# Kernel optimization log

Hardware: AMD Instinct MI355X
Metric: run time of the kernel (lower is better)

Reference implementation:

```python
import jax, jax.numpy as jnp
import numpy as np

B, C, H, W, L = 2, 64, 48, 48, 48
GH, GW, GL = 24, 24, 24  # gating signal at half resolution


def setup_inputs() -> dict:
    key = jax.random.key(0)
    k = jax.random.split(key, 6)
    x = jax.random.normal(k[0], (B, C, H, W, L), dtype=jnp.float32)
    g = jax.random.normal(k[1], (B, C, GH, GW, GL), dtype=jnp.float32)
    s = 1.0 / np.sqrt(C)
    W1 = jax.random.normal(k[2], (C, C), dtype=jnp.float32) * s  # conv1 1x1x1 weight (out,in)
    b1 = jax.random.normal(k[3], (C,), dtype=jnp.float32) * 0.01
    W2 = jax.random.normal(k[4], (C, C), dtype=jnp.float32) * s  # conv2 1x1x1 weight
    b2 = jax.random.normal(k[5], (C,), dtype=jnp.float32) * 0.01
    return {"x": x, "g": g, "W1": W1, "b1": b1, "W2": W2, "b2": b2}


def _conv1x1(v, Wm, b):
    # 1x1x1 Conv3d == channel-mixing matmul
    return jnp.einsum('bchwl,oc->bohwl', v, Wm) + b[None, :, None, None, None]


def reference(x, g, W1, b1, W2, b2):
    theta_x = _conv1x1(x, W1, b1)                       # (B, C, H, W, L)
    theta_g = _conv1x1(g, W2, b2)                       # (B, C, GH, GW, GL)
    # F.upsample(mode='trilinear', align_corners=False) -> half-pixel trilinear resize
    theta_g = jax.image.resize(theta_g, (B, C, H, W, L), method='trilinear')

    # spatially-normalized elementwise gate
    theta_c = theta_x * theta_g
    theta_c = theta_c - jnp.min(theta_c)                # global min over whole tensor
    theta_c = theta_c / jnp.sum(theta_c, axis=(2, 3, 4), keepdims=True)
    p = theta_c * x

    # channel-channel attention per (b,h,w), contracting over L
    theta_c_d = jnp.einsum('bihwl,bjhwl->bhwij', theta_x, theta_g)  # (B,H,W,C,C)
    theta_c_d = theta_c_d - jnp.min(theta_c_d)
    theta_c_d = theta_c_d / jnp.sum(theta_c_d, axis=(1, 2, 3, 4), keepdims=True)
    d = jnp.einsum('bchwl,bhwcj->bjhwl', x, theta_c_d)  # (B, C, H, W, L)
    return (p, d)
```

## Files before the change

### kernel.cpp

```cpp
#include <hip/hip_runtime.h>

#define Bb 2
#define Cc 64
#define Hh 48
#define Ww 48
#define Ll 48
#define HWc (Hh*Ww)
#define HWL (HWc*Ll)
#define GHh 24
#define SG (GHh*GHh*GHh)
#define NBLK (Bb*HWc)
#define CNT1f 110592.0f
#define CNT2f 9437184.0f

__device__ __forceinline__ void interp1(int i, int& a, int& b, float& f){
  float src = i*0.5f - 0.25f;
  float fl = floorf(src);
  f = src - fl;
  int i0 = (int)fl;
  a = i0 < 0 ? 0 : i0;
  int i1 = i0 + 1;
  b = i1 > (GHh-1) ? (GHh-1) : i1;
}

__device__ __forceinline__ void ltaps(int l, int& a, int& b, float& f){
  int i0 = (l - 1) >> 1;
  a = i0 < 0 ? 0 : i0;
  b = i0 + 1 > 23 ? 23 : i0 + 1;
  f = (l & 1) ? 0.25f : 0.75f;
}

__global__ __launch_bounds__(256) void conv_k(const float* __restrict__ in,
    const float* __restrict__ Wm, const float* __restrict__ bias,
    float* __restrict__ out, int S){
  __shared__ __align__(16) float Wl[64][68];
  __shared__ __align__(16) float xl[64][68];
  int t = threadIdx.x;
  int ntile = S >> 6;
  int b  = blockIdx.x / ntile;
  int s0 = (blockIdx.x % ntile) << 6;
  for (int q = t; q < 4096; q += 256){
    int o = q >> 6, c = q & 63;
    Wl[c][o] = Wm[q];
  }
  const float* inb = in + (size_t)b*Cc*S + s0;
  for (int q = t; q < 1024; q += 256){
    int c = q >> 4, v = (q & 15) << 2;
    float4 val = *(const float4*)(inb + (size_t)c*S + v);
    *(float4*)&xl[c][v] = val;
  }
  __syncthreads();
  int o0 = (t & 15) << 2, s1 = (t >> 4) << 2;
  float a00=0,a01=0,a02=0,a03=0,a10=0,a11=0,a12=0,a13=0;
  float a20=0,a21=0,a22=0,a23=0,a30=0,a31=0,a32=0,a33=0;
  #pragma unroll 8
  for (int c = 0; c < 64; ++c){
    float4 wv = *(const float4*)&Wl[c][o0];
    float4 xv = *(const float4*)&xl[c][s1];
    a00 += wv.x*xv.x; a01 += wv.x*xv.y; a02 += wv.x*xv.z; a03 += wv.x*xv.w;
    a10 += wv.y*xv.x; a11 += wv.y*xv.y; a12 += wv.y*xv.z; a13 += wv.y*xv.w;
    a20 += wv.z*xv.x; a21 += wv.z*xv.y; a22 += wv.z*xv.z; a23 += wv.z*xv.w;
    a30 += wv.w*xv.x; a31 += wv.w*xv.y; a32 += wv.w*xv.z; a33 += wv.w*xv.w;
  }
  float* ob = out + (size_t)b*Cc*S + s0 + s1;
  float b0 = bias[o0+0], b1v = bias[o0+1], b2v = bias[o0+2], b3 = bias[o0+3];
  { float4 r = make_float4(a00+b0,a01+b0,a02+b0,a03+b0); *(float4*)(ob + (size_t)(o0+0)*S) = r; }
  { float4 r = make_float4(a10+b1v,a11+b1v,a12+b1v,a13+b1v); *(float4*)(ob + (size_t)(o0+1)*S) = r; }
  { float4 r = make_float4(a20+b2v,a21+b2v,a22+b2v,a23+b2v); *(float4*)(ob + (size_t)(o0+2)*S) = r; }
  { float4 r = make_float4(a30+b3,a31+b3,a32+b3,a33+b3); *(float4*)(ob + (size_t)(o0+3)*S) = r; }
}

__device__ __forceinline__ void g_fold(const float* __restrict__ txt,
    float* __restrict__ G, int t){
  int c = t >> 2, kb = (t & 3)*6;
  const float* T = &txt[c*52];
  #pragma unroll
  for (int i = 0; i < 6; ++i){
    int k = kb + i;
    float v;
    if (k == 0)       v = T[0] + 0.75f*T[1] + 0.25f*T[2];
    else if (k == 23) v = 0.25f*T[45] + 0.75f*T[46] + T[47];
    else              v = 0.25f*T[2*k-1] + 0.75f*T[2*k]
                        + 0.75f*T[2*k+1] + 0.25f*T[2*k+2];
    G[k*68 + c] = v;
  }
}

__device__ __forceinline__ void gather_m(const float* __restrict__ gb,
    float* __restrict__ M, int t, int ha, int hb, int wa, int wb,
    float fh, float fw){
  float omh = 1.f - fh, omw = 1.f - fw;
  for (int u = t; u < 384; u += 256){
    int c = u / 6, s4 = (u % 6) << 2;
    const float* gc = gb + (size_t)c*SG;
    float4 vaa = *(const float4*)(gc + ha*576 + wa*24 + s4);
    float4 vba = *(const float4*)(gc + hb*576 + wa*24 + s4);
    float4 vab = *(const float4*)(gc + ha*576 + wb*24 + s4);
    float4 vbb = *(const float4*)(gc + hb*576 + wb*24 + s4);
    M[(s4+0)*68 + c] = omw*(omh*vaa.x + fh*vba.x) + fw*(omh*vab.x + fh*vbb.x);
    M[(s4+1)*68 + c] = omw*(omh*vaa.y + fh*vba.y) + fw*(omh*vab.y + fh*vbb.y);
    M[(s4+2)*68 + c] = omw*(omh*vaa.z + fh*vba.z) + fw*(omh*vab.z + fh*vbb.z);
    M[(s4+3)*68 + c] = omw*(omh*vaa.w + fh*vba.w) + fw*(omh*vab.w + fh*vbb.w);
  }
}

__global__ __launch_bounds__(256) void reduce_k(const float* __restrict__ tx,
    const float* __restrict__ tgh, float* __restrict__ msite,
    float* __restrict__ gsite, float* __restrict__ part_row,
    float* __restrict__ pm1, float* __restrict__ pm2, float* __restrict__ ps2){
  __shared__ __align__(16) float sh[7224];
  float* txt = sh;
  float* M   = sh + 3328;
  float* G   = sh + 4960;
  float* red = sh + 6592;
  float* CM  = sh + 7104;
  float* SX  = sh + 7128;
  float* sxg = sh + 7176;
  int t = threadIdx.x;
  int bIdx = blockIdx.x;
  int b = bIdx / HWc, hw = bIdx % HWc;
  int h = hw / Ww, w = hw % Ww;
  int ha, hb; float fh; interp1(h, ha, hb, fh);
  int wa, wb; float fw; interp1(w, wa, wb, fw);
  const float* txb = tx + ((size_t)b*Cc*HWc + hw)*Ll;
  #pragma unroll
  for (int k = 0; k < 3; ++k){
    int q = t + (k << 8);
    int c = q / 12, v = (q % 12) << 2;
    *(float4*)&txt[c*52+v] = *(const float4*)(txb + (size_t)c*HWL + v);
  }
  gather_m(tgh + (size_t)b*Cc*SG, M, t, ha, hb, wa, wb, fh, fw);
  __syncthreads();
  g_fold(txt, G, t);
  if (t < 24){
    float s = 0.f;
    #pragma unroll 8
    for (int c = 0; c < 64; ++c) s += M[t*68 + c];
    CM[t] = s;
  }
  if (t >= 192 && t < 240){
    int l = t - 192;
    float s = 0.f;
    #pragma unroll 8
    for (int c = 0; c < 64; ++c) s += txt[c*52 + l];
    SX[l] = s;
  }
  __syncthreads();
  int c = t & 63, lg = t >> 6;
  float pmin = 3.4e38f;
  const float* Trow = &txt[c*52];
  #pragma unroll
  for (int li = 0; li < 12; ++li){
    int l0r = lg*12 + li + c;
    int l = l0r >= 96 ? l0r - 96 : (l0r >= 48 ? l0r - 48 : l0r);
    int la, lb; float fl; ltaps(l, la, lb, fl);
    float tgv = (1.f-fl)*M[la*68 + c] + fl*M[lb*68 + c];
    pmin = fminf(pmin, Trow[l]*tgv);
  }
  if (t < 48){
    int la, lb; float fl; ltaps(t, la, lb, fl);
    sxg[t] = SX[t] * ((1.f-fl)*CM[la] + fl*CM[lb]);
  }
  float* msb = msite + (size_t)bIdx*1536;
  float* gsb = gsite + (size_t)bIdx*1536;
  for (int u = t; u < 384; u += 256){
    int k = u >> 4, c4 = (u & 15) << 2;
    float4 mv;
    mv.x = M[k*68+c4+0]; mv.y = M[k*68+c4+1];
    mv.z = M[k*68+c4+2]; mv.w = M[k*68+c4+3];
    *(float4*)(msb + (u << 2)) = mv;
    float4 gv;
    gv.x = G[k*68+c4+0]; gv.y = G[k*68+c4+1];
    gv.z = G[k*68+c4+2]; gv.w = G[k*68+c4+3];
    *(float4*)(gsb + (u << 2)) = gv;
  }
  int i0 = (t & 15) << 2, j0 = (t >> 4) << 2;
  float a00=0,a01=0,a02=0,a03=0,a10=0,a11=0,a12=0,a13=0;
  float a20=0,a21=0,a22=0,a23=0,a30=0,a31=0,a32=0,a33=0;
  #pragma unroll 4
  for (int k = 0; k < 24; ++k){
    float4 gv = *(const float4*)&G[k*68 + i0];
    float4 mv = *(const float4*)&M[k*68 + j0];
    a00 += gv.x*mv.x; a01 += gv.x*mv.y; a02 += gv.x*mv.z; a03 += gv.x*mv.w;
    a10 += gv.y*mv.x; a11 += gv.y*mv.y; a12 += gv.y*mv.z; a13 += gv.y*mv.w;
    a20 += gv.z*mv.x; a21 += gv.z*mv.y; a22 += gv.z*mv.z; a23 += gv.z*mv.w;
    a30 += gv.w*mv.x; a31 += gv.w*mv.y; a32 += gv.w*mv.z; a33 += gv.w*mv.w;
  }
  float amin = fminf(fminf(fminf(a00,a01),fminf(a02,a03)),
               fminf(fminf(fminf(a10,a11),fminf(a12,a13)),
               fminf(fminf(fminf(a20,a21),fminf(a22,a23)),
                     fminf(fminf(a30,a31),fminf(a32,a33)))));
  if ((t & 15) == (t >> 4)){
    float* pr = part_row + (size_t)bIdx*64 + i0;
    pr[0] = a00; pr[1] = a11; pr[2] = a22; pr[3] = a33;
  }
  red[t] = pmin; red[256+t] = amin;
  __syncthreads();
  if (t < 128){
    red[t] = fminf(red[t], red[t+128]);
    red[256+t] = fminf(red[256+t], red[384+t]);
  }
  __syncthreads();
  if (t < 64){
    float v1 = fminf(red[t], red[t+64]);
    float v2 = fminf(red[256+t], red[320+t]);
    #pragma unroll
    for (int off = 32; off; off >>= 1){
      v1 = fminf(v1, __shfl_down(v1, off));
      v2 = fminf(v2, __shfl_down(v2, off));
    }
    if (t == 0){
      pm1[bIdx] = v1; pm2[bIdx] = v2;
      float tot = 0.f;
      #pragma unroll
      for (int l = 0; l < 48; ++l) tot += sxg[l];
      ps2[bIdx] = tot;
    }
  }
}

__global__ __launch_bounds__(256) void reduce2_k(const float* __restrict__ part_row,
    const float* __restrict__ pm1, const float* __restrict__ pm2,
    const float* __restrict__ ps2, float* __restrict__ rowsum,
    float* __restrict__ gmin, float* __restrict__ s2v){
  __shared__ float red[512];
  int t = threadIdx.x, blk = blockIdx.x;
  if (blk < 128){
    int b = blk >> 6, c = blk & 63;
    const float* src = part_row + (size_t)b*HWc*64 + c;
    float s = 0.f;
    #pragma unroll
    for (int k = 0; k < 9; ++k){
      int i = t + (k << 8);
      s += src[(size_t)i*64];
    }
    red[t] = s; __syncthreads();
    for (int sgap = 128; sgap >= 64; sgap >>= 1){
      if (t < sgap) red[t] += red[t+sgap];
      __syncthreads();
    }
    if (t < 64){
      float v = red[t];
      #pragma unroll
      for (int off = 32; off; off >>= 1) v += __shfl_down(v, off);
      if (t == 0) rowsum[blk] = v;
    }
  } else if (blk == 128){
    float m1 = 3.4e38f, m2 = 3.4e38f;
    for (int i = t; i < NBLK; i += 256){ m1 = fminf(m1, pm1[i]); m2 = fminf(m2, pm2[i]); }
    red[t] = m1; red[256+t] = m2; __syncthreads();
    for (int s = 128; s >= 1; s >>= 1){
      if (t < s){ red[t] = fminf(red[t], red[t+s]); red[256+t] = fminf(red[256+t], red[256+t+s]); }
      __syncthreads();
    }
    if (t == 0){ gmin[0] = red[0]; gmin[1] = red[256]; }
  } else {
    float sa = 0.f, sb = 0.f;
    for (int i = t; i < HWc; i += 256){ sa += ps2[i]; sb += ps2[HWc + i]; }
    red[t] = sa; red[256+t] = sb; __syncthreads();
    for (int s = 128; s >= 1; s >>= 1){
      if (t < s){ red[t] += red[t+s]; red[256+t] += red[256+t+s]; }
      __syncthreads();
    }
    if (t == 0){ s2v[0] = red[0]; s2v[1] = red[256]; }
  }
}

__global__ __launch_bounds__(256) void final_k(const float* __restrict__ x,
    const float* __restrict__ tx, const float* __restrict__ msite,
    const float* __restrict__ gsite, const float* __restrict__ gmin,
    const float* __restrict__ rowsum, const float* __restrict__ s2v,
    float* __restrict__ outp, float* __restrict__ outd){
  __shared__ __align__(16) float sh[7952];
  float* xs  = sh;
  float* M   = sh + 3328;
  float* G   = sh + 4960;
  float* P   = sh + 6592;
  float* iv1 = sh + 7840;
  float* Xs  = sh + 7904;
  int t = threadIdx.x;
  int bIdx = blockIdx.x;
  int b = bIdx / HWc, hw = bIdx % HWc;
  size_t sbase = ((size_t)b*Cc*HWc + hw)*Ll;
  const float* xb  = x  + sbase;
  const float* txb = tx + sbase;
  float m1 = gmin[0], m2 = gmin[1];
  #pragma unroll
  for (int k = 0; k < 3; ++k){
    int q = t + (k << 8);
    int c = q / 12, v = (q % 12) << 2;
    *(float4*)&xs[c*52+v] = *(const float4*)(xb + (size_t)c*HWL + v);
  }
  const float* msb = msite + (size_t)bIdx*1536;
  const float* gsb = gsite + (size_t)bIdx*1536;
  for (int u = t; u < 384; u += 256){
    int k = u >> 4, c4 = (u & 15) << 2;
    *(float4*)&M[k*68 + c4] = *(const float4*)(msb + (u << 2));
    *(float4*)&G[k*68 + c4] = *(const float4*)(gsb + (u << 2));
  }
  if (t < 64) iv1[t] = 1.f/(rowsum[b*64 + t] - m1*CNT1f);
  float invd2 = 1.f/(s2v[b] - m2*CNT2f);
  __syncthreads();
  if (t < 192){
    int k0 = t >> 3, l0 = (t & 7)*6;
    float c0=0,c1=0,c2=0,c3=0,c4=0,c5=0;
    const float* Gr = &G[k0*68];
    #pragma unroll 8
    for (int i = 0; i < 64; ++i){
      float gv = Gr[i];
      const float* xr = &xs[i*52 + l0];
      c0 += gv*xr[0]; c1 += gv*xr[1]; c2 += gv*xr[2];
      c3 += gv*xr[3]; c4 += gv*xr[4]; c5 += gv*xr[5];
    }
    float* pr = &P[k0*52 + l0];
    pr[0]=c0; pr[1]=c1; pr[2]=c2; pr[3]=c3; pr[4]=c4; pr[5]=c5;
  } else if (t < 240){
    int l = t - 192;
    float s = 0.f;
    #pragma unroll 8
    for (int c = 0; c < 64; ++c) s += xs[c*52 + l];
    Xs[l] = s;
  }
  __syncthreads();
  #pragma unroll
  for (int k = 0; k < 3; ++k){
    int q = t + (k << 8);
    int c = q / 12, l4 = (q % 12) << 2;
    int hh = l4 >> 1;
    int im1 = hh - 1 < 0 ? 0 : hh - 1;
    int ip2 = hh + 2 > 23 ? 23 : hh + 2;
    float Mm1 = M[im1*68 + c];
    float M0  = M[hh*68 + c];
    float M1  = M[(hh+1)*68 + c];
    float M2  = M[ip2*68 + c];
    float4 a  = *(const float4*)(txb + (size_t)c*HWL + l4);
    float4 xv = *(const float4*)&xs[c*52 + l4];
    float s = iv1[c];
    float4 r;
    r.x = (a.x*(0.25f*Mm1 + 0.75f*M0) - m1)*s*xv.x;
    r.y = (a.y*(0.75f*M0  + 0.25f*M1) - m1)*s*xv.y;
    r.z = (a.z*(0.25f*M0  + 0.75f*M1) - m1)*s*xv.z;
    r.w = (a.w*(0.75f*M1  + 0.25f*M2) - m1)*s*xv.w;
    *(float4*)(outp + sbase + (size_t)c*HWL + l4) = r;
  }
  __syncthreads();
  {
    int j0 = (t >> 4) << 2, l0 = (t & 15)*3;
    float d00=0,d01=0,d02=0,d10=0,d11=0,d12=0;
    float d20=0,d21=0,d22=0,d30=0,d31=0,d32=0;
    #pragma unroll 4
    for (int k = 0; k < 24; ++k){
      float4 mv = *(const float4*)&M[k*68 + j0];
      const float* pr = &P[k*52 + l0];
      float p0 = pr[0], p1 = pr[1], p2 = pr[2];
      d00 += mv.x*p0; d01 += mv.x*p1; d02 += mv.x*p2;
      d10 += mv.y*p0; d11 += mv.y*p1; d12 += mv.y*p2;
      d20 += mv.z*p0; d21 += mv.z*p1; d22 += mv.z*p2;
      d30 += mv.w*p0; d31 += mv.w*p1; d32 += mv.w*p2;
    }
    float x0 = m2*Xs[l0+0], x1 = m2*Xs[l0+1], x2 = m2*Xs[l0+2];
    float* o0 = outd + sbase + (size_t)(j0+0)*HWL + l0;
    float* o1 = outd + sbase + (size_t)(j0+1)*HWL + l0;
    float* o2 = outd + sbase + (size_t)(j0+2)*HWL + l0;
    float* o3 = outd + sbase + (size_t)(j0+3)*HWL + l0;
    o0[0]=(d00-x0)*invd2; o0[1]=(d01-x1)*invd2; o0[2]=(d02-x2)*invd2;
    o1[0]=(d10-x0)*invd2; o1[1]=(d11-x1)*invd2; o1[2]=(d12-x2)*invd2;
    o2[0]=(d20-x0)*invd2; o2[1]=(d21-x1)*invd2; o2[2]=(d22-x2)*invd2;
    o3[0]=(d30-x0)*invd2; o3[1]=(d31-x1)*invd2; o3[2]=(d32-x2)*invd2;
  }
}

extern "C" void kernel_launch(void* const* d_in, const int* in_sizes, int n_in,
                              void* d_out, int out_size, void* d_ws, size_t ws_size,
                              hipStream_t stream){
  (void)in_sizes; (void)n_in; (void)out_size; (void)ws_size;
  const float* x  = (const float*)d_in[0];
  const float* g  = (const float*)d_in[1];
  const float* W1 = (const float*)d_in[2];
  const float* b1 = (const float*)d_in[3];
  const float* W2 = (const float*)d_in[4];
  const float* b2 = (const float*)d_in[5];
  float* outp = (float*)d_out;
  float* outd = outp + (size_t)Bb*Cc*HWL;
  float* ws   = (float*)d_ws;
  float* txw    = ws;
  float* tghw   = txw + (size_t)Bb*Cc*HWL;
  float* msite  = tghw + (size_t)Bb*Cc*SG;
  float* gsite  = msite + (size_t)NBLK*1536;
  float* part_row = gsite + (size_t)NBLK*1536;
  float* pm1 = part_row + (size_t)NBLK*64;
  float* pm2 = pm1 + NBLK;
  float* ps2 = pm2 + NBLK;
  float* rowsum = ps2 + NBLK;
  float* gmin = rowsum + 128;
  float* s2v  = gmin + 2;

  hipLaunchKernelGGL(conv_k, dim3(Bb*(SG/64)), dim3(256), 0, stream, g, W2, b2, tghw, SG);
  hipLaunchKernelGGL(conv_k, dim3(Bb*(HWL/64)), dim3(256), 0, stream, x, W1, b1, txw, HWL);
  hipLaunchKernelGGL(reduce_k, dim3(NBLK), dim3(256), 0, stream, txw, tghw, msite, gsite,
                     part_row, pm1, pm2, ps2);
  hipLaunchKernelGGL(reduce2_k, dim3(130), dim3(256), 0, stream, part_row, pm1, pm2, ps2,
                     rowsum, gmin, s2v);
  hipLaunchKernelGGL(final_k, dim3(NBLK), dim3(256), 0, stream, x, txw, msite, gsite,
                     gmin, rowsum, s2v, outp, outd);
}
```

Measured before the change: 321.0 us.

## Fuse x 1x1 conv into reduce kernel, computing theta_x per site in shared memory

```diff
diff --git a/kernel.cpp b/kernel.cpp
--- a/kernel.cpp
+++ b/kernel.cpp
@@ -104,40 +104,89 @@
   }
 }
 
-__global__ __launch_bounds__(256) void reduce_k(const float* __restrict__ tx,
-    const float* __restrict__ tgh, float* __restrict__ msite,
-    float* __restrict__ gsite, float* __restrict__ part_row,
-    float* __restrict__ pm1, float* __restrict__ pm2, float* __restrict__ ps2){
-  __shared__ __align__(16) float sh[7224];
+__device__ __forceinline__ void site_conv(const float* __restrict__ xs,
+    const float* __restrict__ Wl, const float* __restrict__ b1,
+    int c0, int l0, float4 acc[4]){
+  acc[0] = make_float4(0.f,0.f,0.f,0.f);
+  acc[1] = make_float4(0.f,0.f,0.f,0.f);
+  acc[2] = make_float4(0.f,0.f,0.f,0.f);
+  acc[3] = make_float4(0.f,0.f,0.f,0.f);
+  #pragma unroll 8
+  for (int cc = 0; cc < 64; ++cc){
+    float4 wv = *(const float4*)&Wl[cc*68 + c0];
+    float4 xv = *(const float4*)&xs[cc*52 + l0];
+    acc[0].x += wv.x*xv.x; acc[0].y += wv.x*xv.y; acc[0].z += wv.x*xv.z; acc[0].w += wv.x*xv.w;
+    acc[1].x += wv.y*xv.x; acc[1].y += wv.y*xv.y; acc[1].z += wv.y*xv.z; acc[1].w += wv.y*xv.w;
+    acc[2].x += wv.z*xv.x; acc[2].y += wv.z*xv.y; acc[2].z += wv.z*xv.z; acc[2].w += wv.z*xv.w;
+    acc[3].x += wv.w*xv.x; acc[3].y += wv.w*xv.y; acc[3].z += wv.w*xv.z; acc[3].w += wv.w*xv.w;
+  }
+  float b0 = b1[c0+0], bb = b1[c0+1], b2 = b1[c0+2], b3 = b1[c0+3];
+  acc[0].x += b0; acc[0].y += b0; acc[0].z += b0; acc[0].w += b0;
+  acc[1].x += bb; acc[1].y += bb; acc[1].z += bb; acc[1].w += bb;
+  acc[2].x += b2; acc[2].y += b2; acc[2].z += b2; acc[2].w += b2;
+  acc[3].x += b3; acc[3].y += b3; acc[3].z += b3; acc[3].w += b3;
+}
+
+__global__ __launch_bounds__(256) void reduce_k(const float* __restrict__ x,
+    const float* __restrict__ W1, const float* __restrict__ b1,
+    const float* __restrict__ tgh, float* __restrict__ txw,
+    float* __restrict__ msite, float* __restrict__ gsite,
+    float* __restrict__ part_row, float* __restrict__ pm1,
+    float* __restrict__ pm2, float* __restrict__ ps2){
+  __shared__ __align__(16) float sh[9312];
   float* txt = sh;
-  float* M   = sh + 3328;
-  float* G   = sh + 4960;
-  float* red = sh + 6592;
-  float* CM  = sh + 7104;
-  float* SX  = sh + 7128;
-  float* sxg = sh + 7176;
+  float* Wl  = sh + 3328;
+  float* G   = sh + 3328;
+  float* red = sh + 4960;
+  float* CM  = sh + 5472;
+  float* SX  = sh + 5496;
+  float* sxg = sh + 5544;
+  float* M   = sh + 7680;
   int t = threadIdx.x;
   int bIdx = blockIdx.x;
   int b = bIdx / HWc, hw = bIdx % HWc;
   int h = hw / Ww, w = hw % Ww;
   int ha, hb; float fh; interp1(h, ha, hb, fh);
   int wa, wb; float fw; interp1(w, wa, wb, fw);
-  const float* txb = tx + ((size_t)b*Cc*HWc + hw)*Ll;
+  const float* xb = x + ((size_t)b*Cc*HWc + hw)*Ll;
   #pragma unroll
   for (int k = 0; k < 3; ++k){
     int q = t + (k << 8);
     int c = q / 12, v = (q % 12) << 2;
-    *(float4*)&txt[c*52+v] = *(const float4*)(txb + (size_t)c*HWL + v);
+    *(float4*)&txt[c*52+v] = *(const float4*)(xb + (size_t)c*HWL + v);
+  }
+  for (int q = t; q < 4096; q += 256){
+    int i = q >> 6, j = q & 63;
+    Wl[i*68 + j] = W1[j*64 + i];
   }
   gather_m(tgh + (size_t)b*Cc*SG, M, t, ha, hb, wa, wb, fh, fw);
   __syncthreads();
+  int c0 = (t & 15) << 2, l0q = (t >> 4) << 2;
+  float4 acc[4];
+  float cmv = 0.f;
+  if (t < 192){
+    site_conv(txt, Wl, b1, c0, l0q, acc);
+  } else if (t < 216){
+    int k = t - 192;
+    #pragma unroll 8
+    for (int c = 0; c < 64; ++c) cmv += M[k*68 + c];
+  }
+  __syncthreads();
+  if (t < 192){
+    *(float4*)&txt[(c0+0)*52 + l0q] = acc[0];
+    *(float4*)&txt[(c0+1)*52 + l0q] = acc[1];
+    *(float4*)&txt[(c0+2)*52 + l0q] = acc[2];
+    *(float4*)&txt[(c0+3)*52 + l0q] = acc[3];
+    float* tb = txw + ((size_t)b*Cc*HWc + hw)*Ll;
+    *(float4*)(tb + (size_t)(c0+0)*HWL + l0q) = acc[0];
+    *(float4*)(tb + (size_t)(c0+1)*HWL + l0q) = acc[1];
+    *(float4*)(tb + (size_t)(c0+2)*HWL + l0q) = acc[2];
+    *(float4*)(tb + (size_t)(c0+3)*HWL + l0q) = acc[3];
+  } else if (t < 216){
+    CM[t-192] = cmv;
+  }
+  __syncthreads();
   g_fold(txt, G, t);
-  if (t < 24){
-    float s = 0.f;
-    #pragma unroll 8
-    for (int c = 0; c < 64; ++c) s += M[t*68 + c];
-    CM[t] = s;
-  }
   if (t >= 192 && t < 240){
     int l = t - 192;
     float s = 0.f;
@@ -396,9 +445,8 @@
   float* s2v  = gmin + 2;
 
   hipLaunchKernelGGL(conv_k, dim3(Bb*(SG/64)), dim3(256), 0, stream, g, W2, b2, tghw, SG);
-  hipLaunchKernelGGL(conv_k, dim3(Bb*(HWL/64)), dim3(256), 0, stream, x, W1, b1, txw, HWL);
-  hipLaunchKernelGGL(reduce_k, dim3(NBLK), dim3(256), 0, stream, txw, tghw, msite, gsite,
-                     part_row, pm1, pm2, ps2);
+  hipLaunchKernelGGL(reduce_k, dim3(NBLK), dim3(256), 0, stream, x, W1, b1, tghw, txw,
+                     msite, gsite, part_row, pm1, pm2, ps2);
   hipLaunchKernelGGL(reduce2_k, dim3(130), dim3(256), 0, stream, part_row, pm1, pm2, ps2,
                      rowsum, gmin, s2v);
   hipLaunchKernelGGL(final_k, dim3(NBLK), dim3(256), 0, stream, x, txw, msite, gsite,
```

Result: no change. 318.6 us (-0.8%).
